# Kernel tuning notes

Measured on AMD Instinct MI355X. Metric: run time of the kernel, lower is better.

The kernel has to match this reference:

```python
import jax, jax.numpy as jnp
import numpy as np

D = 1024
H = 4096  # int(dim * mlp_ratio)
E = 8
B, N = 2, 2048


def setup_inputs() -> dict:
    key = jax.random.key(0)
    ks = jax.random.split(key, 5)
    x = jax.random.normal(ks[0], (B, N, D), dtype=jnp.float32)
    # torch Linear weights, stored pre-transposed for right-multiplication
    W1 = jax.random.normal(ks[1], (E, D, H), dtype=jnp.float32) / np.sqrt(D)
    W2 = jax.random.normal(ks[2], (E, H, D), dtype=jnp.float32) / np.sqrt(H)
    Wg = jax.random.normal(ks[3], (D, E), dtype=jnp.float32) / np.sqrt(D)
    bg = jax.random.normal(ks[4], (E,), dtype=jnp.float32) * 0.01
    return {"x": x, "W1": W1, "W2": W2, "Wg": Wg, "bg": bg}


def reference(x, W1, W2, Wg, bg):
    b, n, d = x.shape
    e = Wg.shape[1]
    xf = x.reshape(b * n, d)                      # [T, D]
    logits = xf @ Wg + bg                         # [T, E]
    one_hot = jax.nn.one_hot(jnp.argmax(logits, axis=-1), e, dtype=x.dtype)  # [T, E]
    # Dense all-experts compute (faithful to the original module)
    h = jax.nn.gelu(jnp.einsum('td,edh->eth', xf, W1), approximate=True)     # [E, T, H]
    y = jnp.einsum('eth,ehd->etd', h, W2)                                    # [E, T, D]
    out = jnp.einsum('etd,te->td', y, one_hot)                               # top-1 combine
    return out.reshape(b, n, d)
```

## Files before the change

kernel.cpp:

```cpp
#include <hip/hip_runtime.h>
#include <hip/hip_bf16.h>

#define Dq 1024
#define Hq 4096
#define Tq 4096
#define MAXTILES 40

#define XB_OFF 65536
#define HC_OFF (XB_OFF + Tq * Dq * 2)
#define WT_OFF (HC_OFF + MAXTILES * 128 * Hq * 2)

#define M_NT 0
#define M_CNT 8
#define M_POFF 16
#define M_CUR 32
#define M_TE 64
#define M_TR 128
#define M_EXP 512
#define M_PERM 4608

typedef __attribute__((ext_vector_type(8))) short bf16x8;
typedef __attribute__((ext_vector_type(4))) float f32x4;

__device__ __forceinline__ short f2bf(float f) {
    __hip_bfloat16 h = __float2bfloat16(f);
    return *reinterpret_cast<short*>(&h);
}

__device__ __forceinline__ float gelu_tanh(float x) {
    float u = 0.7978845608028654f * (x + 0.044715f * x * x * x);
    return x / (1.0f + __expf(-2.0f * u));
}

typedef __attribute__((address_space(1))) const void gvoid;
typedef __attribute__((address_space(3))) void lvoid;
__device__ __forceinline__ void glds16(const void* g, void* l) {
    __builtin_amdgcn_global_load_lds((gvoid*)g, (lvoid*)l, 16, 0, 0);
}

#define WAITVM_(N) asm volatile("s_waitcnt vmcnt(" #N ")" ::: "memory")
#define WAITVM(N) WAITVM_(N)

__global__ void k_init(int* meta) {
    int i = blockIdx.x * 256 + threadIdx.x;
    if (i < M_PERM + MAXTILES * 128) meta[i] = 0;
}

__global__ void k_tr(const float* __restrict__ in, short* __restrict__ out, int R, int C) {
    __shared__ float t[64][65];
    int e = blockIdx.z;
    int c0 = blockIdx.x * 64;
    int r0 = blockIdx.y * 64;
    const float* ine = in + (size_t)e * R * C;
    short* oute = out + (size_t)e * R * C;
    int tt = threadIdx.x;
    int lr = tt >> 4;
    int lc = (tt & 15) * 4;
#pragma unroll
    for (int p = 0; p < 4; ++p) {
        int r = p * 16 + lr;
        float4 v = *(const float4*)(ine + (size_t)(r0 + r) * C + c0 + lc);
        t[r][lc] = v.x; t[r][lc + 1] = v.y; t[r][lc + 2] = v.z; t[r][lc + 3] = v.w;
    }
    __syncthreads();
#pragma unroll
    for (int p = 0; p < 4; ++p) {
        int c = p * 16 + lr;
        short4 s;
        s.x = f2bf(t[lc][c]); s.y = f2bf(t[lc + 1][c]);
        s.z = f2bf(t[lc + 2][c]); s.w = f2bf(t[lc + 3][c]);
        *(short4*)(oute + (size_t)(c0 + c) * R + r0 + lc) = s;
    }
}

__global__ void k_route(const float* __restrict__ x, const float* __restrict__ Wg,
                        const float* __restrict__ bg, int* meta, short* __restrict__ xb) {
    int wave = threadIdx.x >> 6;
    int lane = threadIdx.x & 63;
    int t = blockIdx.x * 4 + wave;
    const float* xr = x + (size_t)t * Dq;
    float acc[8];
#pragma unroll
    for (int e = 0; e < 8; ++e) acc[e] = 0.0f;
#pragma unroll
    for (int j = 0; j < 16; ++j) {
        int d = j * 64 + lane;
        float xv = xr[d];
        xb[(size_t)t * Dq + d] = f2bf(xv);
        float4 w0 = *(const float4*)(Wg + (size_t)d * 8);
        float4 w1 = *(const float4*)(Wg + (size_t)d * 8 + 4);
        acc[0] += xv * w0.x; acc[1] += xv * w0.y; acc[2] += xv * w0.z; acc[3] += xv * w0.w;
        acc[4] += xv * w1.x; acc[5] += xv * w1.y; acc[6] += xv * w1.z; acc[7] += xv * w1.w;
    }
#pragma unroll
    for (int e = 0; e < 8; ++e) {
#pragma unroll
        for (int off = 32; off > 0; off >>= 1) acc[e] += __shfl_xor(acc[e], off);
    }
    if (lane == 0) {
        float best = acc[0] + bg[0];
        int be = 0;
#pragma unroll
        for (int e = 1; e < 8; ++e) {
            float v = acc[e] + bg[e];
            if (v > best) { best = v; be = e; }
        }
        meta[M_EXP + t] = be;
        atomicAdd(&meta[M_CNT + be], 1);
    }
}

__global__ void k_scan(int* meta) {
    if (threadIdx.x != 0) return;
    int off = 0, nt = 0;
    for (int e = 0; e < 8; ++e) {
        meta[M_POFF + e] = off;
        int c = meta[M_CNT + e];
        int m = (c + 127) / 128;
        for (int j = 0; j < m; ++j) {
            meta[M_TE + nt] = e;
            meta[M_TR + nt] = off + j * 128;
            ++nt;
        }
        off += m * 128;
    }
    meta[M_POFF + 8] = off;
    meta[M_NT] = nt;
}

__global__ void k_scatter(int* meta) {
    int t = blockIdx.x * 256 + threadIdx.x;
    if (t >= Tq) return;
    int e = meta[M_EXP + t];
    int pos = atomicAdd(&meta[M_CUR + e], 1);
    meta[M_PERM + meta[M_POFF + e] + pos] = t;
}

#define GEMM_SETUP()                                                           \
    int tt = threadIdx.x, w = tt >> 6, lane = tt & 63;                         \
    int fr = lane & 15, fg = lane >> 4;                                        \
    int rlo = lane >> 3;                                                       \
    int csw = ((lane & 7) ^ rlo) * 8;                                          \
    int ldsOff[4];                                                             \
    _Pragma("unroll")                                                          \
    for (int s = 0; s < 4; ++s) ldsOff[s] = (s * 32 + w * 8) * 64;             \
    int wm = (w >> 1) * 64, wn = (w & 1) * 64;                                 \
    int aoff[2][4], boff[2][4];                                                \
    _Pragma("unroll")                                                          \
    for (int s2 = 0; s2 < 2; ++s2)                                             \
      _Pragma("unroll")                                                        \
      for (int f = 0; f < 4; ++f) {                                            \
        int c = s2 * 4 + fg;                                                   \
        int m = wm + f * 16 + fr;                                              \
        aoff[s2][f] = m * 64 + ((c ^ (m & 7)) * 8);                            \
        int n = wn + f * 16 + fr;                                              \
        boff[s2][f] = n * 64 + ((c ^ (n & 7)) * 8);                            \
      }                                                                        \
    f32x4 acc[4][4];                                                           \
    _Pragma("unroll")                                                          \
    for (int a = 0; a < 4; ++a)                                                \
      _Pragma("unroll")                                                        \
      for (int b = 0; b < 2 * 2; ++b) acc[a][b] = (f32x4){0.f, 0.f, 0.f, 0.f};

#define PHASE(S2, P)                                                           \
  {                                                                            \
    bf16x8 af[4], bv[4];                                                       \
    _Pragma("unroll")                                                          \
    for (int f = 0; f < 4; ++f) {                                              \
      af[f] = *(const bf16x8*)(&As[(P) * 8192 + aoff[S2][f]]);                 \
      bv[f] = *(const bf16x8*)(&Bs[(P) * 8192 + boff[S2][f]]);                 \
    }                                                                          \
    __builtin_amdgcn_s_barrier();                                              \
    asm volatile("s_waitcnt lgkmcnt(0)" ::: "memory");                         \
    __builtin_amdgcn_sched_barrier(0);                                         \
    __builtin_amdgcn_s_setprio(1);                                             \
    _Pragma("unroll")                                                          \
    for (int fm = 0; fm < 4; ++fm)                                             \
      _Pragma("unroll")                                                        \
      for (int fn = 0; fn < 4; ++fn)                                           \
        acc[fm][fn] = __builtin_amdgcn_mfma_f32_16x16x32_bf16(                 \
            af[fm], bv[fn], acc[fm][fn], 0, 0, 0);                             \
    __builtin_amdgcn_s_setprio(0);                                             \
    __builtin_amdgcn_s_barrier();                                              \
    asm volatile("" ::: "memory");                                             \
  }

#define KSTEP(T, NSTEP)                                                        \
  {                                                                            \
    const int P = (T) & 1;                                                     \
    if ((T) + 1 < (NSTEP)) {                                                   \
      _Pragma("unroll")                                                        \
      for (int s = 0; s < 4; ++s) {                                            \
        glds16(aSrc[s] + ((T) + 1) * 64, As + (1 - P) * 8192 + ldsOff[s]);     \
        glds16(bSrc[s] + ((T) + 1) * 64, Bs + (1 - P) * 8192 + ldsOff[s]);     \
      }                                                                        \
      WAITVM(8);                                                               \
    } else {                                                                   \
      WAITVM(0);                                                               \
    }                                                                          \
    __builtin_amdgcn_s_barrier();                                              \
    asm volatile("" ::: "memory");                                             \
    PHASE(0, P)                                                                \
    PHASE(1, P)                                                                \
  }

__global__ __launch_bounds__(256, 2) void k_gemm1(const short* __restrict__ xb,
                                                  const short* __restrict__ W1T,
                                                  const int* __restrict__ meta,
                                                  short* __restrict__ Hc) {
    __shared__ short As[2 * 8192];
    __shared__ short Bs[2 * 8192];
    int hw = blockIdx.x;
    int xcd = hw & 7, q = hw >> 3;
    int mt = q % 40;
    int n0 = (xcd * 4 + q / 40) * 128;
    if (mt >= meta[M_NT]) return;
    int e = meta[M_TE + mt];
    int i0 = meta[M_TR + mt];
    const int* perm = meta + M_PERM;

    GEMM_SETUP()

    const short* aSrc[4];
    const short* bSrc[4];
#pragma unroll
    for (int s = 0; s < 4; ++s) {
        int row = s * 32 + w * 8 + rlo;
        aSrc[s] = xb + (size_t)perm[i0 + row] * Dq + csw;
        bSrc[s] = W1T + ((size_t)e * Hq + n0 + row) * Dq + csw;
    }

#pragma unroll
    for (int s = 0; s < 4; ++s) {
        glds16(aSrc[s], As + ldsOff[s]);
        glds16(bSrc[s], Bs + ldsOff[s]);
    }

#pragma unroll 2
    for (int t = 0; t < 16; ++t) KSTEP(t, 16)

#pragma unroll
    for (int fm = 0; fm < 4; ++fm) {
        int rbase = i0 + wm + fm * 16 + fg * 4;
#pragma unroll
        for (int fn = 0; fn < 4; ++fn) {
            int col = n0 + wn + fn * 16 + fr;
#pragma unroll
            for (int p = 0; p < 4; ++p) {
                float v = gelu_tanh(acc[fm][fn][p]);
                Hc[(size_t)(rbase + p) * Hq + col] = f2bf(v);
            }
        }
    }
}

__global__ __launch_bounds__(256, 2) void k_gemm2(const short* __restrict__ Hc,
                                                  const short* __restrict__ W2T,
                                                  const int* __restrict__ meta,
                                                  float* __restrict__ out) {
    __shared__ short As[2 * 8192];
    __shared__ short Bs[2 * 8192];
    int hw = blockIdx.x;
    int xcd = hw & 7, q = hw >> 3;
    int mt = q >> 1;
    int sk = q & 1;
    int n0 = xcd * 128;
    int kbase = sk * (Hq / 2);
    if (mt >= meta[M_NT]) return;
    int e = meta[M_TE + mt];
    int i0 = meta[M_TR + mt];
    const int* perm = meta + M_PERM;
    int vend = meta[M_POFF + e] + meta[M_CNT + e];

    GEMM_SETUP()

    const short* aSrc[4];
    const short* bSrc[4];
#pragma unroll
    for (int s = 0; s < 4; ++s) {
        int row = s * 32 + w * 8 + rlo;
        aSrc[s] = Hc + (size_t)(i0 + row) * Hq + kbase + csw;
        bSrc[s] = W2T + ((size_t)e * Dq + n0 + row) * Hq + kbase + csw;
    }

#pragma unroll
    for (int s = 0; s < 4; ++s) {
        glds16(aSrc[s], As + ldsOff[s]);
        glds16(bSrc[s], Bs + ldsOff[s]);
    }

#pragma unroll 2
    for (int t = 0; t < 32; ++t) KSTEP(t, 32)

#pragma unroll
    for (int fm = 0; fm < 4; ++fm) {
        int rbase = i0 + wm + fm * 16 + fg * 4;
#pragma unroll
        for (int p = 0; p < 4; ++p) {
            int i = rbase + p;
            if (i < vend) {
                int tok = perm[i];
#pragma unroll
                for (int fn = 0; fn < 4; ++fn) {
                    int col = n0 + wn + fn * 16 + fr;
                    atomicAdd(&out[(size_t)tok * Dq + col], acc[fm][fn][p]);
                }
            }
        }
    }
}

extern "C" void kernel_launch(void* const* d_in, const int* in_sizes, int n_in,
                              void* d_out, int out_size, void* d_ws, size_t ws_size,
                              hipStream_t stream) {
    const float* x  = (const float*)d_in[0];
    const float* W1 = (const float*)d_in[1];
    const float* W2 = (const float*)d_in[2];
    const float* Wg = (const float*)d_in[3];
    const float* bg = (const float*)d_in[4];
    float* out = (float*)d_out;
    int* meta = (int*)d_ws;
    short* xb = (short*)((char*)d_ws + XB_OFF);
    short* Hc = (short*)((char*)d_ws + HC_OFF);
    short* WT = (short*)((char*)d_ws + WT_OFF);

    k_init<<<38, 256, 0, stream>>>(meta);
    hipMemsetAsync(d_out, 0, (size_t)Tq * Dq * 4, stream);
    k_route<<<Tq / 4, 256, 0, stream>>>(x, Wg, bg, meta, xb);
    k_scan<<<1, 64, 0, stream>>>(meta);
    k_scatter<<<Tq / 256, 256, 0, stream>>>(meta);
    k_tr<<<dim3(Hq / 64, Dq / 64, 8), 256, 0, stream>>>(W1, WT, Dq, Hq);
    k_gemm1<<<1280, 256, 0, stream>>>(xb, WT, meta, Hc);
    k_tr<<<dim3(Dq / 64, Hq / 64, 8), 256, 0, stream>>>(W2, WT, Hq, Dq);
    k_gemm2<<<640, 256, 0, stream>>>(Hc, WT, meta, out);
}
```

Baseline: 310.0 us.

## Use 256-row expert tiles with 512-thread blocks and triple-buffered LDS pipeline

Both expert GEMMs now use 256x128 output tiles. Each 512-thread block has 8 waves, and the token dimension is padded to multiples of 256 per expert. Global-to-LDS loads go through a three-stage ring buffer that prefetches two k-steps ahead, with vmcnt waits adjusted to match. The aim is more operand reuse per weight tile and better hiding of load latency. In exchange, each block uses much more LDS, which caps occupancy, and coarser padding adds wasted rows per expert.

Result: slower. 337.8 us (+9.0%).

```diff
diff --git a/kernel.cpp b/kernel.cpp
--- a/kernel.cpp
+++ b/kernel.cpp
@@ -4,11 +4,11 @@
 #define Dq 1024
 #define Hq 4096
 #define Tq 4096
-#define MAXTILES 40
+#define MAXT2 24
 
 #define XB_OFF 65536
 #define HC_OFF (XB_OFF + Tq * Dq * 2)
-#define WT_OFF (HC_OFF + MAXTILES * 128 * Hq * 2)
+#define WT_OFF (HC_OFF + MAXT2 * 256 * Hq * 2)
 
 #define M_NT 0
 #define M_CNT 8
@@ -43,7 +43,7 @@
 
 __global__ void k_init(int* meta) {
     int i = blockIdx.x * 256 + threadIdx.x;
-    if (i < M_PERM + MAXTILES * 128) meta[i] = 0;
+    if (i < M_PERM + MAXT2 * 256) meta[i] = 0;
 }
 
 __global__ void k_tr(const float* __restrict__ in, short* __restrict__ out, int R, int C) {
@@ -116,13 +116,13 @@
     for (int e = 0; e < 8; ++e) {
         meta[M_POFF + e] = off;
         int c = meta[M_CNT + e];
-        int m = (c + 127) / 128;
+        int m = (c + 255) / 256;
         for (int j = 0; j < m; ++j) {
             meta[M_TE + nt] = e;
-            meta[M_TR + nt] = off + j * 128;
+            meta[M_TR + nt] = off + j * 256;
             ++nt;
         }
-        off += m * 128;
+        off += m * 256;
     }
     meta[M_POFF + 8] = off;
     meta[M_NT] = nt;
@@ -141,9 +141,11 @@
     int fr = lane & 15, fg = lane >> 4;                                        \
     int rlo = lane >> 3;                                                       \
     int csw = ((lane & 7) ^ rlo) * 8;                                          \
-    int ldsOff[4];                                                             \
-    _Pragma("unroll")                                                          \
-    for (int s = 0; s < 4; ++s) ldsOff[s] = (s * 32 + w * 8) * 64;             \
+    int ldsA[4], ldsB[2];                                                      \
+    _Pragma("unroll")                                                          \
+    for (int i = 0; i < 4; ++i) ldsA[i] = (i * 8 + w) * 512;                   \
+    _Pragma("unroll")                                                          \
+    for (int i = 0; i < 2; ++i) ldsB[i] = (i * 8 + w) * 512;                   \
     int wm = (w >> 1) * 64, wn = (w & 1) * 64;                                 \
     int aoff[2][4], boff[2][4];                                                \
     _Pragma("unroll")                                                          \
@@ -160,15 +162,25 @@
     _Pragma("unroll")                                                          \
     for (int a = 0; a < 4; ++a)                                                \
       _Pragma("unroll")                                                        \
-      for (int b = 0; b < 2 * 2; ++b) acc[a][b] = (f32x4){0.f, 0.f, 0.f, 0.f};
-
-#define PHASE(S2, P)                                                           \
+      for (int b = 0; b < 4; ++b) acc[a][b] = (f32x4){0.f, 0.f, 0.f, 0.f};
+
+#define STAGE(T, BUF)                                                          \
+  {                                                                            \
+    _Pragma("unroll")                                                          \
+    for (int i = 0; i < 4; ++i)                                                \
+      glds16(aSrc[i] + (size_t)(T) * 64, As + (BUF) * 16384 + ldsA[i]);        \
+    _Pragma("unroll")                                                          \
+    for (int i = 0; i < 2; ++i)                                                \
+      glds16(bSrc[i] + (size_t)(T) * 64, Bs + (BUF) * 8192 + ldsB[i]);         \
+  }
+
+#define PHASE(S2, BUF)                                                         \
   {                                                                            \
     bf16x8 af[4], bv[4];                                                       \
     _Pragma("unroll")                                                          \
     for (int f = 0; f < 4; ++f) {                                              \
-      af[f] = *(const bf16x8*)(&As[(P) * 8192 + aoff[S2][f]]);                 \
-      bv[f] = *(const bf16x8*)(&Bs[(P) * 8192 + boff[S2][f]]);                 \
+      af[f] = *(const bf16x8*)(&As[(BUF) * 16384 + aoff[S2][f]]);              \
+      bv[f] = *(const bf16x8*)(&Bs[(BUF) * 8192 + boff[S2][f]]);               \
     }                                                                          \
     __builtin_amdgcn_s_barrier();                                              \
     asm volatile("s_waitcnt lgkmcnt(0)" ::: "memory");                         \
@@ -187,33 +199,31 @@
 
 #define KSTEP(T, NSTEP)                                                        \
   {                                                                            \
-    const int P = (T) & 1;                                                     \
-    if ((T) + 1 < (NSTEP)) {                                                   \
-      _Pragma("unroll")                                                        \
-      for (int s = 0; s < 4; ++s) {                                            \
-        glds16(aSrc[s] + ((T) + 1) * 64, As + (1 - P) * 8192 + ldsOff[s]);     \
-        glds16(bSrc[s] + ((T) + 1) * 64, Bs + (1 - P) * 8192 + ldsOff[s]);     \
-      }                                                                        \
-      WAITVM(8);                                                               \
+    const int BUF = (T) % 3;                                                   \
+    if ((T) + 2 < (NSTEP)) {                                                   \
+      STAGE((T) + 2, ((T) + 2) % 3)                                            \
+      WAITVM(12);                                                              \
+    } else if ((T) + 2 == (NSTEP)) {                                           \
+      WAITVM(6);                                                               \
     } else {                                                                   \
       WAITVM(0);                                                               \
     }                                                                          \
     __builtin_amdgcn_s_barrier();                                              \
     asm volatile("" ::: "memory");                                             \
-    PHASE(0, P)                                                                \
-    PHASE(1, P)                                                                \
+    PHASE(0, BUF)                                                              \
+    PHASE(1, BUF)                                                              \
   }
 
-__global__ __launch_bounds__(256, 2) void k_gemm1(const short* __restrict__ xb,
+__global__ __launch_bounds__(512, 2) void k_gemm1(const short* __restrict__ xb,
                                                   const short* __restrict__ W1T,
                                                   const int* __restrict__ meta,
                                                   short* __restrict__ Hc) {
-    __shared__ short As[2 * 8192];
-    __shared__ short Bs[2 * 8192];
+    __shared__ short As[3 * 16384];
+    __shared__ short Bs[3 * 8192];
     int hw = blockIdx.x;
     int xcd = hw & 7, q = hw >> 3;
-    int mt = q % 40;
-    int n0 = (xcd * 4 + q / 40) * 128;
+    int mt = q % MAXT2;
+    int n0 = (xcd * 4 + q / MAXT2) * 128;
     if (mt >= meta[M_NT]) return;
     int e = meta[M_TE + mt];
     int i0 = meta[M_TR + mt];
@@ -222,21 +232,22 @@
     GEMM_SETUP()
 
     const short* aSrc[4];
-    const short* bSrc[4];
-#pragma unroll
-    for (int s = 0; s < 4; ++s) {
-        int row = s * 32 + w * 8 + rlo;
-        aSrc[s] = xb + (size_t)perm[i0 + row] * Dq + csw;
-        bSrc[s] = W1T + ((size_t)e * Hq + n0 + row) * Dq + csw;
-    }
-
-#pragma unroll
-    for (int s = 0; s < 4; ++s) {
-        glds16(aSrc[s], As + ldsOff[s]);
-        glds16(bSrc[s], Bs + ldsOff[s]);
-    }
-
-#pragma unroll 2
+    const short* bSrc[2];
+#pragma unroll
+    for (int i = 0; i < 4; ++i) {
+        int row = (i * 8 + w) * 8 + rlo;
+        aSrc[i] = xb + (size_t)perm[i0 + row] * Dq + csw;
+    }
+#pragma unroll
+    for (int i = 0; i < 2; ++i) {
+        int row = (i * 8 + w) * 8 + rlo;
+        bSrc[i] = W1T + ((size_t)e * Hq + n0 + row) * Dq + csw;
+    }
+
+    STAGE(0, 0)
+    STAGE(1, 1)
+
+#pragma unroll
     for (int t = 0; t < 16; ++t) KSTEP(t, 16)
 
 #pragma unroll
@@ -254,16 +265,16 @@
     }
 }
 
-__global__ __launch_bounds__(256, 2) void k_gemm2(const short* __restrict__ Hc,
+__global__ __launch_bounds__(512, 2) void k_gemm2(const short* __restrict__ Hc,
                                                   const short* __restrict__ W2T,
                                                   const int* __restrict__ meta,
                                                   float* __restrict__ out) {
-    __shared__ short As[2 * 8192];
-    __shared__ short Bs[2 * 8192];
+    __shared__ short As[3 * 16384];
+    __shared__ short Bs[3 * 8192];
     int hw = blockIdx.x;
     int xcd = hw & 7, q = hw >> 3;
+    int sk = q & 1;
     int mt = q >> 1;
-    int sk = q & 1;
     int n0 = xcd * 128;
     int kbase = sk * (Hq / 2);
     if (mt >= meta[M_NT]) return;
@@ -275,21 +286,22 @@
     GEMM_SETUP()
 
     const short* aSrc[4];
-    const short* bSrc[4];
-#pragma unroll
-    for (int s = 0; s < 4; ++s) {
-        int row = s * 32 + w * 8 + rlo;
-        aSrc[s] = Hc + (size_t)(i0 + row) * Hq + kbase + csw;
-        bSrc[s] = W2T + ((size_t)e * Dq + n0 + row) * Hq + kbase + csw;
-    }
-
-#pragma unroll
-    for (int s = 0; s < 4; ++s) {
-        glds16(aSrc[s], As + ldsOff[s]);
-        glds16(bSrc[s], Bs + ldsOff[s]);
-    }
-
-#pragma unroll 2
+    const short* bSrc[2];
+#pragma unroll
+    for (int i = 0; i < 4; ++i) {
+        int row = (i * 8 + w) * 8 + rlo;
+        aSrc[i] = Hc + (size_t)(i0 + row) * Hq + kbase + csw;
+    }
+#pragma unroll
+    for (int i = 0; i < 2; ++i) {
+        int row = (i * 8 + w) * 8 + rlo;
+        bSrc[i] = W2T + ((size_t)e * Dq + n0 + row) * Hq + kbase + csw;
+    }
+
+    STAGE(0, 0)
+    STAGE(1, 1)
+
+#pragma unroll
     for (int t = 0; t < 32; ++t) KSTEP(t, 32)
 
 #pragma unroll
@@ -324,13 +336,13 @@
     short* Hc = (short*)((char*)d_ws + HC_OFF);
     short* WT = (short*)((char*)d_ws + WT_OFF);
 
-    k_init<<<38, 256, 0, stream>>>(meta);
+    k_init<<<48, 256, 0, stream>>>(meta);
     hipMemsetAsync(d_out, 0, (size_t)Tq * Dq * 4, stream);
     k_route<<<Tq / 4, 256, 0, stream>>>(x, Wg, bg, meta, xb);
     k_scan<<<1, 64, 0, stream>>>(meta);
     k_scatter<<<Tq / 256, 256, 0, stream>>>(meta);
     k_tr<<<dim3(Hq / 64, Dq / 64, 8), 256, 0, stream>>>(W1, WT, Dq, Hq);
-    k_gemm1<<<1280, 256, 0, stream>>>(xb, WT, meta, Hc);
+    k_gemm1<<<768, 512, 0, stream>>>(xb, WT, meta, Hc);
     k_tr<<<dim3(Dq / 64, Hq / 64, 8), 256, 0, stream>>>(W2, WT, Hq, Dq);
-    k_gemm2<<<640, 256, 0, stream>>>(Hc, WT, meta, out);
-}
+    k_gemm2<<<384, 512, 0, stream>>>(Hc, WT, meta, out);
+}
```

## Use wave-private LDS tiles to drop block barriers in expert GEMMs

Applied to the files above, without the earlier changes.

Each wave now stages its own 64-row slices of A and B into a private LDS region with a new swizzle and a K step of 32. This removes all block-wide s_barriers and the setprio calls from the GEMM main loops. The cost is that waves sharing rows now load the same global data twice, roughly doubling L2 and global traffic, and the smaller K step doubles the loop iteration count. The gemm2 grid mapping is also reordered so that the split-K halves are grouped by tile index.

After: 379.0 us. +22.3%, slower.

```diff
diff --git a/kernel.cpp b/kernel.cpp
--- a/kernel.cpp
+++ b/kernel.cpp
@@ -139,69 +139,55 @@
 #define GEMM_SETUP()                                                           \
     int tt = threadIdx.x, w = tt >> 6, lane = tt & 63;                         \
     int fr = lane & 15, fg = lane >> 4;                                        \
-    int rlo = lane >> 3;                                                       \
-    int csw = ((lane & 7) ^ rlo) * 8;                                          \
-    int ldsOff[4];                                                             \
+    int r16 = lane >> 2;                                                       \
+    int csw = ((lane & 3) ^ ((lane >> 3) & 3)) * 8;                            \
+    int ldsW = w * 2048;                                                       \
+    int wm = (w >> 1) * 64, wn = (w & 1) * 64;                                 \
+    int aoff[4], boff[4];                                                      \
     _Pragma("unroll")                                                          \
-    for (int s = 0; s < 4; ++s) ldsOff[s] = (s * 32 + w * 8) * 64;             \
-    int wm = (w >> 1) * 64, wn = (w & 1) * 64;                                 \
-    int aoff[2][4], boff[2][4];                                                \
-    _Pragma("unroll")                                                          \
-    for (int s2 = 0; s2 < 2; ++s2)                                             \
-      _Pragma("unroll")                                                        \
-      for (int f = 0; f < 4; ++f) {                                            \
-        int c = s2 * 4 + fg;                                                   \
-        int m = wm + f * 16 + fr;                                              \
-        aoff[s2][f] = m * 64 + ((c ^ (m & 7)) * 8);                            \
-        int n = wn + f * 16 + fr;                                              \
-        boff[s2][f] = n * 64 + ((c ^ (n & 7)) * 8);                            \
-      }                                                                        \
+    for (int f = 0; f < 4; ++f) {                                              \
+        int row = f * 16 + fr;                                                 \
+        int sw = (fg ^ ((row >> 1) & 3)) * 8;                                  \
+        aoff[f] = ldsW + row * 32 + sw;                                        \
+        boff[f] = ldsW + row * 32 + sw;                                        \
+    }                                                                          \
     f32x4 acc[4][4];                                                           \
     _Pragma("unroll")                                                          \
     for (int a = 0; a < 4; ++a)                                                \
       _Pragma("unroll")                                                        \
-      for (int b = 0; b < 2 * 2; ++b) acc[a][b] = (f32x4){0.f, 0.f, 0.f, 0.f};
-
-#define PHASE(S2, P)                                                           \
-  {                                                                            \
+      for (int b = 0; b < 4; ++b) acc[a][b] = (f32x4){0.f, 0.f, 0.f, 0.f};
+
+#define KLOOP(NS)                                                              \
+  _Pragma("unroll 2")                                                          \
+  for (int t = 0; t < (NS); ++t) {                                             \
+    const int P = t & 1;                                                       \
+    if (t + 1 < (NS)) {                                                        \
+      _Pragma("unroll")                                                        \
+      for (int s = 0; s < 4; ++s)                                              \
+        glds16(aSrc[s] + (size_t)(t + 1) * 32,                                 \
+               As + (1 - P) * 8192 + ldsW + s * 512);                          \
+      _Pragma("unroll")                                                        \
+      for (int s = 0; s < 4; ++s)                                              \
+        glds16(bSrc[s] + (size_t)(t + 1) * 32,                                 \
+               Bs + (1 - P) * 8192 + ldsW + s * 512);                          \
+      WAITVM(8);                                                               \
+    } else {                                                                   \
+      WAITVM(0);                                                               \
+    }                                                                          \
     bf16x8 af[4], bv[4];                                                       \
     _Pragma("unroll")                                                          \
     for (int f = 0; f < 4; ++f) {                                              \
-      af[f] = *(const bf16x8*)(&As[(P) * 8192 + aoff[S2][f]]);                 \
-      bv[f] = *(const bf16x8*)(&Bs[(P) * 8192 + boff[S2][f]]);                 \
+      af[f] = *(const bf16x8*)(&As[P * 8192 + aoff[f]]);                       \
+      bv[f] = *(const bf16x8*)(&Bs[P * 8192 + boff[f]]);                       \
     }                                                                          \
-    __builtin_amdgcn_s_barrier();                                              \
     asm volatile("s_waitcnt lgkmcnt(0)" ::: "memory");                         \
     __builtin_amdgcn_sched_barrier(0);                                         \
-    __builtin_amdgcn_s_setprio(1);                                             \
     _Pragma("unroll")                                                          \
     for (int fm = 0; fm < 4; ++fm)                                             \
       _Pragma("unroll")                                                        \
       for (int fn = 0; fn < 4; ++fn)                                           \
         acc[fm][fn] = __builtin_amdgcn_mfma_f32_16x16x32_bf16(                 \
             af[fm], bv[fn], acc[fm][fn], 0, 0, 0);                             \
-    __builtin_amdgcn_s_setprio(0);                                             \
-    __builtin_amdgcn_s_barrier();                                              \
-    asm volatile("" ::: "memory");                                             \
-  }
-
-#define KSTEP(T, NSTEP)                                                        \
-  {                                                                            \
-    const int P = (T) & 1;                                                     \
-    if ((T) + 1 < (NSTEP)) {                                                   \
-      _Pragma("unroll")                                                        \
-      for (int s = 0; s < 4; ++s) {                                            \
-        glds16(aSrc[s] + ((T) + 1) * 64, As + (1 - P) * 8192 + ldsOff[s]);     \
-        glds16(bSrc[s] + ((T) + 1) * 64, Bs + (1 - P) * 8192 + ldsOff[s]);     \
-      }                                                                        \
-      WAITVM(8);                                                               \
-    } else {                                                                   \
-      WAITVM(0);                                                               \
-    }                                                                          \
-    __builtin_amdgcn_s_barrier();                                              \
-    asm volatile("" ::: "memory");                                             \
-    PHASE(0, P)                                                                \
-    PHASE(1, P)                                                                \
   }
 
 __global__ __launch_bounds__(256, 2) void k_gemm1(const short* __restrict__ xb,
@@ -225,19 +211,19 @@
     const short* bSrc[4];
 #pragma unroll
     for (int s = 0; s < 4; ++s) {
-        int row = s * 32 + w * 8 + rlo;
-        aSrc[s] = xb + (size_t)perm[i0 + row] * Dq + csw;
-        bSrc[s] = W1T + ((size_t)e * Hq + n0 + row) * Dq + csw;
+        int arow = wm + s * 16 + r16;
+        aSrc[s] = xb + (size_t)perm[i0 + arow] * Dq + csw;
+        int brow = wn + s * 16 + r16;
+        bSrc[s] = W1T + ((size_t)e * Hq + n0 + brow) * Dq + csw;
     }
 
 #pragma unroll
     for (int s = 0; s < 4; ++s) {
-        glds16(aSrc[s], As + ldsOff[s]);
-        glds16(bSrc[s], Bs + ldsOff[s]);
-    }
-
-#pragma unroll 2
-    for (int t = 0; t < 16; ++t) KSTEP(t, 16)
+        glds16(aSrc[s], As + ldsW + s * 512);
+        glds16(bSrc[s], Bs + ldsW + s * 512);
+    }
+
+    KLOOP(32)
 
 #pragma unroll
     for (int fm = 0; fm < 4; ++fm) {
@@ -262,8 +248,8 @@
     __shared__ short Bs[2 * 8192];
     int hw = blockIdx.x;
     int xcd = hw & 7, q = hw >> 3;
-    int mt = q >> 1;
-    int sk = q & 1;
+    int mt = q % 40;
+    int sk = q / 40;
     int n0 = xcd * 128;
     int kbase = sk * (Hq / 2);
     if (mt >= meta[M_NT]) return;
@@ -278,19 +264,19 @@
     const short* bSrc[4];
 #pragma unroll
     for (int s = 0; s < 4; ++s) {
-        int row = s * 32 + w * 8 + rlo;
-        aSrc[s] = Hc + (size_t)(i0 + row) * Hq + kbase + csw;
-        bSrc[s] = W2T + ((size_t)e * Dq + n0 + row) * Hq + kbase + csw;
+        int arow = wm + s * 16 + r16;
+        aSrc[s] = Hc + (size_t)(i0 + arow) * Hq + kbase + csw;
+        int brow = wn + s * 16 + r16;
+        bSrc[s] = W2T + ((size_t)e * Dq + n0 + brow) * Hq + kbase + csw;
     }
 
 #pragma unroll
     for (int s = 0; s < 4; ++s) {
-        glds16(aSrc[s], As + ldsOff[s]);
-        glds16(bSrc[s], Bs + ldsOff[s]);
-    }
-
-#pragma unroll 2
-    for (int t = 0; t < 32; ++t) KSTEP(t, 32)
+        glds16(aSrc[s], As + ldsW + s * 512);
+        glds16(bSrc[s], Bs + ldsW + s * 512);
+    }
+
+    KLOOP(64)
 
 #pragma unroll
     for (int fm = 0; fm < 4; ++fm) {
```
